# Optimization experiments

Hardware: AMD Instinct MI355X
Metric: run time of the kernel (lower is better)

Reference implementation:

```python
import jax, jax.numpy as jnp
import numpy as np

DIM = 2048
HEAD_DIM = 128
N_HEADS = 16
N_KV = 4
THETA = 10000.0
M = 2
B = 2
S = 2048


def _rope_table(seq_len, head_dim, theta):
    half = head_dim // 2
    inv_freq = 1.0 / (theta ** (jnp.arange(half, dtype=jnp.float32) * 2.0 / head_dim))
    ang = jnp.outer(jnp.arange(seq_len, dtype=jnp.float32), inv_freq)  # [S, half]
    cos, sin = jnp.cos(ang), jnp.sin(ang)
    # [S, half, 2, 2] rotation matrices: [[cos, -sin], [sin, cos]]
    return jnp.stack([jnp.stack([cos, -sin], axis=-1), jnp.stack([sin, cos], axis=-1)], axis=-2)


def setup_inputs() -> dict:
    key = jax.random.key(0)
    ks = jax.random.split(key, 6)
    std = DIM ** -0.5
    x = jax.random.normal(ks[0], (B, S, DIM), jnp.float32)
    Wq = jax.random.normal(ks[1], (M, DIM, N_HEADS * HEAD_DIM), jnp.float32) * std
    Wk = jax.random.normal(ks[2], (M, M, DIM, N_KV * HEAD_DIM), jnp.float32) * std
    Wv = jax.random.normal(ks[3], (M, M, DIM, N_KV * HEAD_DIM), jnp.float32) * std
    Wo = jax.random.normal(ks[4], (M, N_HEADS * HEAD_DIM, DIM), jnp.float32) * std
    modality_ids = jax.random.randint(ks[5], (B, S), 0, M, dtype=jnp.int32)
    freq_cis = _rope_table(S, HEAD_DIM, THETA)
    return {"x": x, "freq_cis": freq_cis, "Wq": Wq, "Wk": Wk, "Wv": Wv, "Wo": Wo,
            "modality_ids": modality_ids}


def _select_by_modality(all_proj, mid):
    # all_proj: [B, S, M, E]; mid: [B, S] int -> [B, S, E]
    Bb, Ss, Mm, E = all_proj.shape
    idx = jnp.broadcast_to(mid[:, :, None, None].astype(jnp.int32), (Bb, Ss, 1, E))
    return jnp.take_along_axis(all_proj, idx, axis=2)[:, :, 0]


def reference(x, freq_cis, Wq, Wk, Wv, Wo, modality_ids):
    Bb, Ss, D = x.shape
    mid = modality_ids

    # Per-modality Q projection, then per-token selection (gather/scatter in torch).
    q_all = jnp.einsum('bsd,mde->bsme', x, Wq)  # [B,S,M,H*hd]
    xq = _select_by_modality(q_all, mid)

    # In the original, xk[src token] accumulates wk[src_to_tgt](x) over ALL tgt,
    # which by linearity equals x @ sum_tgt(Wk[src, tgt]).
    Wk_sum = Wk.sum(axis=1)  # [M, D, Kh*hd]
    Wv_sum = Wv.sum(axis=1)
    k_all = jnp.einsum('bsd,mde->bsme', x, Wk_sum)
    v_all = jnp.einsum('bsd,mde->bsme', x, Wv_sum)
    xk = _select_by_modality(k_all, mid)
    xv = _select_by_modality(v_all, mid)

    xq = xq.reshape(Bb, Ss, N_HEADS, HEAD_DIM)
    xk = xk.reshape(Bb, Ss, N_KV, HEAD_DIM)
    xv = xv.reshape(Bb, Ss, N_KV, HEAD_DIM)

    # RoPE (positions = arange since tok_idx is None)
    F = freq_cis[:Ss]  # [S, hd/2, 2, 2]

    def rope(t):
        th = t.reshape(t.shape[0], t.shape[1], t.shape[2], HEAD_DIM // 2, 2)
        return jnp.einsum('bshdp,sdpq->bshdq', th, F).reshape(t.shape)

    xq = rope(xq)
    xk = rope(xk)

    # GQA repeat (interleaved, matching expand+reshape)
    rep = N_HEADS // N_KV
    xk = jnp.repeat(xk, rep, axis=2)
    xv = jnp.repeat(xv, rep, axis=2)

    q = xq.transpose(0, 2, 1, 3)  # [B,H,S,hd]
    k = xk.transpose(0, 2, 1, 3)
    v = xv.transpose(0, 2, 1, 3)

    scale = 1.0 / jnp.sqrt(jnp.asarray(HEAD_DIM, dtype=q.dtype))
    scores = jnp.einsum('bhqd,bhkd->bhqk', q, k) * scale
    attn = jax.nn.softmax(scores, axis=-1)
    out = jnp.einsum('bhqk,bhkd->bqhd', attn, v).reshape(Bb, Ss, N_HEADS * HEAD_DIM)

    # Per-modality output projection + selection
    o_all = jnp.einsum('bse,med->bsmd', out, Wo)  # [B,S,M,D]
    final = _select_by_modality(o_all, mid)
    return final
```

## Files before the change

kernel.cpp:

```cpp
#include <hip/hip_runtime.h>
#include <hip/hip_bf16.h>
#include <stdint.h>

typedef unsigned short u16;
typedef __attribute__((ext_vector_type(8))) __bf16 bf16x8;
typedef __attribute__((ext_vector_type(4))) float f32x4;
typedef __attribute__((ext_vector_type(16))) float f32x16;
typedef __attribute__((ext_vector_type(8))) u16 us8;
typedef __attribute__((ext_vector_type(4))) unsigned u32x4;

#define QSCALE 0.08838834764831843f

__device__ __forceinline__ u16 f2bf(float f) {
  unsigned u = __float_as_uint(f);
  u += 0x7fffu + ((u >> 16) & 1u);
  return (u16)(u >> 16);
}
__device__ __forceinline__ float bf2f(u16 h) {
  return __uint_as_float(((unsigned)h) << 16);
}
__device__ __forceinline__ void gload16(const void* g, void* l) {
  __builtin_amdgcn_global_load_lds(
      (const __attribute__((address_space(1))) unsigned int*)g,
      (__attribute__((address_space(3))) unsigned int*)l, 16, 0, 0);
}
__device__ __forceinline__ unsigned sx32(unsigned v) {
  return (unsigned)__shfl_xor((int)v, 32, 64);
}

__global__ __launch_bounds__(256) void wprep(
    const float* __restrict__ Wq, const float* __restrict__ Wk,
    const float* __restrict__ Wv, const float* __restrict__ Wo,
    u16* __restrict__ WCT, u16* __restrict__ WOT) {
  const int sec = blockIdx.z;
  const float* s0;
  const float* s1 = nullptr;
  u16* dst;
  int N;
  switch (sec) {
    case 0: s0 = Wq;                 dst = WCT;               N = 2048; break;
    case 1: s0 = Wq + 2048*2048;     dst = WCT + 2048*2048;   N = 2048; break;
    case 2: s0 = Wk;                 s1 = Wk + 2048*512;      dst = WCT + 4096*2048; N = 512; break;
    case 3: s0 = Wk + 2*2048*512;    s1 = Wk + 3*2048*512;    dst = WCT + 4608*2048; N = 512; break;
    case 4: s0 = Wv;                 s1 = Wv + 2048*512;      dst = WCT + 5120*2048; N = 512; break;
    case 5: s0 = Wv + 2*2048*512;    s1 = Wv + 3*2048*512;    dst = WCT + 5632*2048; N = 512; break;
    case 6: s0 = Wo;                 dst = WOT;               N = 2048; break;
    default: s0 = Wo + 2048*2048;    dst = WOT + 2048*2048;   N = 2048; break;
  }
  const int n0 = blockIdx.x * 32;
  if (n0 >= N) return;
  const int k0 = blockIdx.y * 32;
  __shared__ float tile[32][33];
  const int tx = threadIdx.x & 31, ty = threadIdx.x >> 5;
#pragma unroll
  for (int i = 0; i < 4; ++i) {
    int k = k0 + ty + 8 * i;
    float v = s0[(size_t)k * N + n0 + tx];
    if (s1) v += s1[(size_t)k * N + n0 + tx];
    tile[ty + 8 * i][tx] = v;
  }
  __syncthreads();
#pragma unroll
  for (int i = 0; i < 4; ++i) {
    int n = n0 + ty + 8 * i;
    dst[(size_t)n * 2048 + k0 + tx] = f2bf(tile[tx][ty + 8 * i]);
  }
}

__global__ __launch_bounds__(256) void xcast(const float* __restrict__ x,
                                             u16* __restrict__ Xbf) {
  size_t base = ((size_t)blockIdx.x * 256 + threadIdx.x) * 8;
  float4 a = *(const float4*)&x[base];
  float4 c = *(const float4*)&x[base + 4];
  us8 o;
  o[0] = f2bf(a.x); o[1] = f2bf(a.y); o[2] = f2bf(a.z); o[3] = f2bf(a.w);
  o[4] = f2bf(c.x); o[5] = f2bf(c.y); o[6] = f2bf(c.z); o[7] = f2bf(c.w);
  *(us8*)&Xbf[base] = o;
}

__global__ __launch_bounds__(256) void gemm_bt(
    const u16* __restrict__ A, const u16* __restrict__ B, u16* __restrict__ C,
    int Mdim, int Ndim, int Kdim) {
  __shared__ u16 As[128 * 32];
  __shared__ u16 Bs[128 * 32];
  const int nbx = gridDim.x;
  const int nwg = nbx * gridDim.y;
  int bid = blockIdx.y * nbx + blockIdx.x;
  const int q = nwg >> 3;
  int swz = (bid & 7) * q + (bid >> 3);
  const int bx = swz % nbx, by = swz / nbx;
  const int row0 = by * 128, col0 = bx * 128;
  const int tid = threadIdx.x, wid = tid >> 6, lane = tid & 63;
  const int lr = lane & 15, lg = lane >> 4;
  const int wr = wid >> 1, wc = wid & 1;
  const u16* Abase = A + (size_t)row0 * Kdim;
  const u16* Bbase = B + (size_t)col0 * Kdim;

  f32x4 acc[4][4];
#pragma unroll
  for (int m = 0; m < 4; ++m)
#pragma unroll
    for (int n = 0; n < 4; ++n)
#pragma unroll
      for (int r = 0; r < 4; ++r) acc[m][n][r] = 0.f;

  for (int k0 = 0; k0 < Kdim; k0 += 32) {
#pragma unroll
    for (int j = 0; j < 2; ++j) {
      int c = j * 256 + wid * 64 + lane;
      int r = c >> 2, g = c & 3;
      gload16(Abase + (size_t)r * Kdim + k0 + g * 8, &As[(j * 256 + wid * 64) * 8]);
      gload16(Bbase + (size_t)r * Kdim + k0 + g * 8, &Bs[(j * 256 + wid * 64) * 8]);
    }
    __syncthreads();
    bf16x8 af[4], bfr[4];
#pragma unroll
    for (int m = 0; m < 4; ++m)
      af[m] = *(const bf16x8*)&As[(64 * wr + 16 * m + lr) * 32 + 8 * lg];
#pragma unroll
    for (int n = 0; n < 4; ++n)
      bfr[n] = *(const bf16x8*)&Bs[(64 * wc + 16 * n + lr) * 32 + 8 * lg];
#pragma unroll
    for (int m = 0; m < 4; ++m)
#pragma unroll
      for (int n = 0; n < 4; ++n)
        acc[m][n] = __builtin_amdgcn_mfma_f32_16x16x32_bf16(af[m], bfr[n], acc[m][n], 0, 0, 0);
    __syncthreads();
  }
#pragma unroll
  for (int m = 0; m < 4; ++m)
#pragma unroll
    for (int n = 0; n < 4; ++n)
#pragma unroll
      for (int r = 0; r < 4; ++r) {
        int grow = row0 + 64 * wr + 16 * m + 4 * lg + r;
        int gcol = col0 + 64 * wc + 16 * n + lr;
        C[(size_t)grow * Ndim + gcol] = f2bf(acc[m][n][r]);
      }
}

__global__ __launch_bounds__(256) void gemm_out(
    const u16* __restrict__ A, const u16* __restrict__ B,
    const int* __restrict__ mid, float* __restrict__ out) {
  __shared__ u16 As[128 * 32];
  __shared__ u16 Bs[128 * 32];
  const int nbx = gridDim.x;
  const int nwg = nbx * gridDim.y;
  int bid = blockIdx.y * nbx + blockIdx.x;
  const int q = nwg >> 3;
  int swz = (bid & 7) * q + (bid >> 3);
  const int bx = swz % nbx, by = swz / nbx;
  const int row0 = by * 128, col0 = bx * 128;
  const int tid = threadIdx.x, wid = tid >> 6, lane = tid & 63;
  const int lr = lane & 15, lg = lane >> 4;
  const int wr = wid >> 1, wc = wid & 1;
  const u16* Abase = A + (size_t)row0 * 2048;
  const u16* Bbase = B + (size_t)col0 * 2048;

  f32x4 acc[4][4];
#pragma unroll
  for (int m = 0; m < 4; ++m)
#pragma unroll
    for (int n = 0; n < 4; ++n)
#pragma unroll
      for (int r = 0; r < 4; ++r) acc[m][n][r] = 0.f;

  for (int k0 = 0; k0 < 2048; k0 += 32) {
#pragma unroll
    for (int j = 0; j < 2; ++j) {
      int c = j * 256 + wid * 64 + lane;
      int r = c >> 2, g = c & 3;
      gload16(Abase + (size_t)r * 2048 + k0 + g * 8, &As[(j * 256 + wid * 64) * 8]);
      gload16(Bbase + (size_t)r * 2048 + k0 + g * 8, &Bs[(j * 256 + wid * 64) * 8]);
    }
    __syncthreads();
    bf16x8 af[4], bfr[4];
#pragma unroll
    for (int m = 0; m < 4; ++m)
      af[m] = *(const bf16x8*)&As[(64 * wr + 16 * m + lr) * 32 + 8 * lg];
#pragma unroll
    for (int n = 0; n < 4; ++n)
      bfr[n] = *(const bf16x8*)&Bs[(64 * wc + 16 * n + lr) * 32 + 8 * lg];
#pragma unroll
    for (int m = 0; m < 4; ++m)
#pragma unroll
      for (int n = 0; n < 4; ++n)
        acc[m][n] = __builtin_amdgcn_mfma_f32_16x16x32_bf16(af[m], bfr[n], acc[m][n], 0, 0, 0);
    __syncthreads();
  }
#pragma unroll
  for (int m = 0; m < 4; ++m)
#pragma unroll
    for (int n = 0; n < 4; ++n)
#pragma unroll
      for (int r = 0; r < 4; ++r) {
        int grow = row0 + 64 * wr + 16 * m + 4 * lg + r;
        int gcol = col0 + 64 * wc + 16 * n + lr;
        int mod = gcol >> 11;
        if (mid[grow] == mod)
          out[(size_t)grow * 2048 + (gcol & 2047)] = acc[m][n][r];
      }
}

__global__ __launch_bounds__(256) void rope_select(
    const u16* __restrict__ QKV, const int* __restrict__ mid,
    const float* __restrict__ fc, u16* __restrict__ Qr, u16* __restrict__ Kr) {
  const int t = blockIdx.x;
  const int b = t >> 11, s = t & 2047;
  const int m = mid[t];
  __shared__ float Fs[256];
  Fs[threadIdx.x] = fc[(size_t)s * 256 + threadIdx.x];
  __syncthreads();
  const int tid = threadIdx.x;
  {
    int p0 = tid * 4;
    int h = p0 >> 6, ph0 = p0 & 63;
    const u16* src = QKV + (size_t)t * 6144 + m * 2048 + h * 128 + 2 * ph0;
    us8 v = *(const us8*)src;
    us8 o;
#pragma unroll
    for (int j = 0; j < 4; ++j) {
      float x0 = bf2f(v[2 * j]), x1 = bf2f(v[2 * j + 1]);
      const float* F = &Fs[(ph0 + j) * 4];
      o[2 * j]     = f2bf((x0 * F[0] + x1 * F[2]) * QSCALE);
      o[2 * j + 1] = f2bf((x0 * F[1] + x1 * F[3]) * QSCALE);
    }
    *(us8*)(Qr + (((size_t)(b * 16 + h) * 2048) + s) * 128 + 2 * ph0) = o;
  }
  if (tid < 64) {
    int p0 = tid * 4;
    int kh = p0 >> 6, ph0 = p0 & 63;
    const u16* src = QKV + (size_t)t * 6144 + 4096 + m * 512 + kh * 128 + 2 * ph0;
    us8 v = *(const us8*)src;
    us8 o;
#pragma unroll
    for (int j = 0; j < 4; ++j) {
      float x0 = bf2f(v[2 * j]), x1 = bf2f(v[2 * j + 1]);
      const float* F = &Fs[(ph0 + j) * 4];
      o[2 * j]     = f2bf(x0 * F[0] + x1 * F[2]);
      o[2 * j + 1] = f2bf(x0 * F[1] + x1 * F[3]);
    }
    *(us8*)(Kr + (((size_t)(b * 4 + kh) * 2048) + s) * 128 + 2 * ph0) = o;
  }
}

__global__ __launch_bounds__(256) void vtrans(
    const u16* __restrict__ QKV, const int* __restrict__ mid, u16* __restrict__ Vt) {
  __shared__ u16 tilebuf[32][34];
  const int s0 = blockIdx.x * 32, d0 = blockIdx.y * 32, b = blockIdx.z;
  const int tx = threadIdx.x & 31, ty = threadIdx.x >> 5;
#pragma unroll
  for (int i = 0; i < 4; ++i) {
    int s = s0 + ty + 8 * i;
    int t = b * 2048 + s;
    int m = mid[t];
    tilebuf[ty + 8 * i][tx] = QKV[(size_t)t * 6144 + 5120 + m * 512 + d0 + tx];
  }
  __syncthreads();
#pragma unroll
  for (int i = 0; i < 4; ++i) {
    int d = d0 + ty + 8 * i;
    Vt[(((size_t)(b * 4 + (d >> 7)) * 128) + (d & 127)) * 2048 + s0 + tx] =
        tilebuf[tx][ty + 8 * i];
  }
}

__global__ __launch_bounds__(512, 2) void attn(
    const u16* __restrict__ Qr, const u16* __restrict__ Kr,
    const u16* __restrict__ Vt, u16* __restrict__ AO) {
  __shared__ u16 smem[34816];
  u16* Kbuf[2] = { smem,          smem + 16384 };
  u16* Vbuf[2] = { smem +  8192,  smem + 24576 };
  Kbuf[0] = smem;          Vbuf[0] = smem + 8192;
  Kbuf[1] = smem + 16384;  Vbuf[1] = smem + 24576;

  const int qt = blockIdx.x, hd = blockIdx.y, b = blockIdx.z;
  const int kvh = hd >> 2;
  const int tid = threadIdx.x, wid = tid >> 6;
  const int l31 = tid & 31, h = (tid >> 5) & 1;
  const bool hi = h != 0;

  const u16* qp = Qr + (((size_t)(b * 16 + hd) * 2048) + qt * 256 + wid * 32 + l31) * 128;
  const u16* kp = Kr + ((size_t)(b * 4 + kvh) * 2048) * 128;
  const u16* vp = Vt + ((size_t)(b * 4 + kvh) * 128) * 2048;

  bf16x8 qf[8];
#pragma unroll
  for (int ds = 0; ds < 8; ++ds)
    qf[ds] = *(const bf16x8*)(qp + 16 * ds + 8 * h);

  f32x16 oacc[4];
#pragma unroll
  for (int dt = 0; dt < 4; ++dt)
#pragma unroll
    for (int r = 0; r < 16; ++r) oacc[dt][r] = 0.f;
  float mrun = -1e30f, lrun = 0.f;

#define STAGE_KV(KB, DK, DV)                                                   \
  {                                                                            \
    _Pragma("unroll") for (int j = 0; j < 2; ++j) {                            \
      int c = j * 512 + tid;                                                   \
      int rk = c >> 4, gk = (c & 15) ^ (rk & 7);                               \
      gload16(kp + (size_t)((KB) + rk) * 128 + gk * 8,                         \
              (DK) + (j * 512 + wid * 64) * 8);                                \
      int rv = c >> 3, gv = (c & 7) ^ (rv & 7);                                \
      gload16(vp + (size_t)rv * 2048 + (KB) + gv * 8,                          \
              (DV) + (j * 512 + wid * 64) * 8);                                \
    }                                                                          \
  }

  STAGE_KV(0, Kbuf[0], Vbuf[0]);
  __syncthreads();

  int cur = 0;
  for (int kb = 0; kb < 2048; kb += 64) {
    const u16* Kb = Kbuf[cur];
    const u16* Vb = Vbuf[cur];
    if (kb + 64 < 2048) STAGE_KV(kb + 64, Kbuf[cur ^ 1], Vbuf[cur ^ 1]);

    f32x16 s0, s1;
#pragma unroll
    for (int r = 0; r < 16; ++r) { s0[r] = 0.f; s1[r] = 0.f; }
    const int key0 = l31, key1 = 32 + l31;
#pragma unroll
    for (int ds = 0; ds < 8; ++ds) {
      bf16x8 kf0 = *(const bf16x8*)&Kb[key0 * 128 + (((2 * ds + h) ^ (key0 & 7)) * 8)];
      s0 = __builtin_amdgcn_mfma_f32_32x32x16_bf16(kf0, qf[ds], s0, 0, 0, 0);
      bf16x8 kf1 = *(const bf16x8*)&Kb[key1 * 128 + (((2 * ds + h) ^ (key1 & 7)) * 8)];
      s1 = __builtin_amdgcn_mfma_f32_32x32x16_bf16(kf1, qf[ds], s1, 0, 0, 0);
    }

    float pm = -1e30f;
#pragma unroll
    for (int r = 0; r < 16; ++r) pm = fmaxf(pm, fmaxf(s0[r], s1[r]));
    pm = fmaxf(pm, __shfl_xor(pm, 32, 64));
    if (!__all(pm <= mrun + 8.f)) {
      float mn = fmaxf(mrun, pm);
      float sc = __expf(mrun - mn);
      mrun = mn;
      lrun *= sc;
#pragma unroll
      for (int dt = 0; dt < 4; ++dt)
#pragma unroll
        for (int r = 0; r < 16; ++r) oacc[dt][r] *= sc;
    }
    float ls = 0.f;
#pragma unroll
    for (int r = 0; r < 16; ++r) { s0[r] = __expf(s0[r] - mrun); ls += s0[r]; }
#pragma unroll
    for (int r = 0; r < 16; ++r) { s1[r] = __expf(s1[r] - mrun); ls += s1[r]; }
    ls += __shfl_xor(ls, 32, 64);
    lrun += ls;

    unsigned c[16];
#pragma unroll
    for (int j = 0; j < 8; ++j) {
      asm("v_cvt_pk_bf16_f32 %0, %1, %2" : "=v"(c[j]) : "v"(s0[2 * j]), "v"(s0[2 * j + 1]));
      asm("v_cvt_pk_bf16_f32 %0, %1, %2" : "=v"(c[8 + j]) : "v"(s1[2 * j]), "v"(s1[2 * j + 1]));
    }

#pragma unroll
    for (int st = 0; st < 4; ++st) {
      unsigned w0 = sx32(c[4 * st + 0]);
      unsigned w1 = sx32(c[4 * st + 1]);
      unsigned w2 = sx32(c[4 * st + 2]);
      unsigned w3 = sx32(c[4 * st + 3]);
      u32x4 pw;
      pw.x = hi ? w2 : c[4 * st + 0];
      pw.y = hi ? w3 : c[4 * st + 1];
      pw.z = hi ? c[4 * st + 2] : w0;
      pw.w = hi ? c[4 * st + 3] : w1;
      union { u32x4 u; bf16x8 bf; } pc;
      pc.u = pw;
#pragma unroll
      for (int dt = 0; dt < 4; ++dt) {
        int d = 32 * dt + l31;
        bf16x8 vf = *(const bf16x8*)&Vb[d * 64 + (((2 * st + h) ^ (d & 7)) * 8)];
        oacc[dt] = __builtin_amdgcn_mfma_f32_32x32x16_bf16(vf, pc.bf, oacc[dt], 0, 0, 0);
      }
    }
    __syncthreads();
    cur ^= 1;
  }

  u16* Os = smem;
  const float inv = 1.0f / lrun;
  const int q = wid * 32 + l31;
#pragma unroll
  for (int dt = 0; dt < 4; ++dt)
#pragma unroll
    for (int a = 0; a < 4; ++a) {
      int d = 32 * dt + 8 * a + 4 * h;
      ushort4 w;
      w.x = f2bf(oacc[dt][4 * a + 0] * inv);
      w.y = f2bf(oacc[dt][4 * a + 1] * inv);
      w.z = f2bf(oacc[dt][4 * a + 2] * inv);
      w.w = f2bf(oacc[dt][4 * a + 3] * inv);
      *(ushort4*)&Os[q * 136 + d] = w;
    }
  __syncthreads();
  const size_t orow = (size_t)b * 2048 + qt * 256;
#pragma unroll
  for (int rep = 0; rep < 8; ++rep) {
    int idx = rep * 512 + tid;
    int qq = idx >> 4, g = idx & 15;
    us8 v = *(const us8*)&Os[qq * 136 + g * 8];
    *(us8*)&AO[(orow + qq) * 2048 + hd * 128 + g * 8] = v;
  }
#undef STAGE_KV
}

extern "C" void kernel_launch(void* const* d_in, const int* in_sizes, int n_in,
                              void* d_out, int out_size, void* d_ws, size_t ws_size,
                              hipStream_t stream) {
  const float* x  = (const float*)d_in[0];
  const float* fc = (const float*)d_in[1];
  const float* Wq = (const float*)d_in[2];
  const float* Wk = (const float*)d_in[3];
  const float* Wv = (const float*)d_in[4];
  const float* Wo = (const float*)d_in[5];
  const int* mid  = (const int*)d_in[6];
  float* out = (float*)d_out;
  char* ws = (char*)d_ws;

  u16* XBF = (u16*)(ws);
  u16* WCT = (u16*)(ws + 16777216);
  u16* WOT = (u16*)(ws + 41943040);
  u16* QKV = (u16*)(ws + 58720256);
  u16* QR  = (u16*)(ws + 109051904);
  u16* KR  = (u16*)(ws + 125829120);
  u16* VT  = (u16*)(ws + 130023424);
  u16* AO  = (u16*)(ws + 134217728);
  if (ws_size < 150994944) return;

  wprep<<<dim3(64, 64, 8), dim3(256), 0, stream>>>(Wq, Wk, Wv, Wo, WCT, WOT);
  xcast<<<dim3(4096), dim3(256), 0, stream>>>(x, XBF);
  gemm_bt<<<dim3(48, 32), dim3(256), 0, stream>>>(XBF, WCT, QKV, 4096, 6144, 2048);
  rope_select<<<dim3(4096), dim3(256), 0, stream>>>(QKV, mid, fc, QR, KR);
  vtrans<<<dim3(64, 16, 2), dim3(256), 0, stream>>>(QKV, mid, VT);
  attn<<<dim3(8, 16, 2), dim3(512), 0, stream>>>(QR, KR, VT, AO);
  gemm_out<<<dim3(32, 32), dim3(256), 0, stream>>>(AO, WOT, mid, out);
}
```

Before: 540.0 us.

## Group tokens by modality and run only the matching projection per token

Adds count and scatter kernels that build a permutation sorting tokens by modality, then gathers rows through that permutation so each token is multiplied only by its own modality's Q/K/V and output weights. This halves GEMM FLOPs and the size of the QKV intermediate compared with computing every modality and discarding the unused one. The costs are two small extra launches, an atomic-based scatter, indirect row loads, and up to one partially empty tile per segment. Rope, V transpose and the output store now index through the permutation.

```diff
diff --git a/kernel.cpp b/kernel.cpp
--- a/kernel.cpp
+++ b/kernel.cpp
@@ -38,14 +38,14 @@
   u16* dst;
   int N;
   switch (sec) {
-    case 0: s0 = Wq;                 dst = WCT;               N = 2048; break;
-    case 1: s0 = Wq + 2048*2048;     dst = WCT + 2048*2048;   N = 2048; break;
-    case 2: s0 = Wk;                 s1 = Wk + 2048*512;      dst = WCT + 4096*2048; N = 512; break;
-    case 3: s0 = Wk + 2*2048*512;    s1 = Wk + 3*2048*512;    dst = WCT + 4608*2048; N = 512; break;
-    case 4: s0 = Wv;                 s1 = Wv + 2048*512;      dst = WCT + 5120*2048; N = 512; break;
-    case 5: s0 = Wv + 2*2048*512;    s1 = Wv + 3*2048*512;    dst = WCT + 5632*2048; N = 512; break;
-    case 6: s0 = Wo;                 dst = WOT;               N = 2048; break;
-    default: s0 = Wo + 2048*2048;    dst = WOT + 2048*2048;   N = 2048; break;
+    case 0: s0 = Wq;                 dst = WCT;                    N = 2048; break;
+    case 1: s0 = Wq + 2048*2048;     dst = WCT + (size_t)3072*2048; N = 2048; break;
+    case 2: s0 = Wk;                 s1 = Wk + 2048*512;  dst = WCT + (size_t)2048*2048; N = 512; break;
+    case 3: s0 = Wk + 2*2048*512;    s1 = Wk + 3*2048*512; dst = WCT + (size_t)5120*2048; N = 512; break;
+    case 4: s0 = Wv;                 s1 = Wv + 2048*512;  dst = WCT + (size_t)2560*2048; N = 512; break;
+    case 5: s0 = Wv + 2*2048*512;    s1 = Wv + 3*2048*512; dst = WCT + (size_t)5632*2048; N = 512; break;
+    case 6: s0 = Wo;                 dst = WOT;                    N = 2048; break;
+    default: s0 = Wo + 2048*2048;    dst = WOT + (size_t)2048*2048; N = 2048; break;
   }
   const int n0 = blockIdx.x * 32;
   if (n0 >= N) return;
@@ -78,23 +78,59 @@
   *(us8*)&Xbf[base] = o;
 }
 
-__global__ __launch_bounds__(256) void gemm_bt(
-    const u16* __restrict__ A, const u16* __restrict__ B, u16* __restrict__ C,
-    int Mdim, int Ndim, int Kdim) {
+__global__ __launch_bounds__(256) void scount(const int* __restrict__ mid,
+                                              int* __restrict__ cnt) {
+  __shared__ int sh[256];
+  int s = 0;
+  for (int i = threadIdx.x; i < 4096; i += 256) s += (mid[i] == 0);
+  sh[threadIdx.x] = s;
+  __syncthreads();
+  for (int o = 128; o; o >>= 1) {
+    if (threadIdx.x < o) sh[threadIdx.x] += sh[threadIdx.x + o];
+    __syncthreads();
+  }
+  if (threadIdx.x == 0) { cnt[0] = sh[0]; cnt[1] = 0; cnt[2] = 0; }
+}
+
+__global__ __launch_bounds__(256) void sscatter(const int* __restrict__ mid,
+                                                int* __restrict__ cnt,
+                                                int* __restrict__ perm,
+                                                int* __restrict__ inv) {
+  int t = blockIdx.x * 256 + threadIdx.x;
+  int m = mid[t];
+  int base = m ? cnt[0] : 0;
+  int pos = base + atomicAdd(&cnt[1 + m], 1);
+  perm[pos] = t;
+  inv[t] = pos;
+}
+
+__global__ __launch_bounds__(256) void gemm_qkv(
+    const u16* __restrict__ A, const u16* __restrict__ W, u16* __restrict__ Cq,
+    const int* __restrict__ cnt, const int* __restrict__ perm) {
   __shared__ u16 As[128 * 32];
   __shared__ u16 Bs[128 * 32];
-  const int nbx = gridDim.x;
-  const int nwg = nbx * gridDim.y;
+  const int n0 = cnt[0];
+  const int nbx = 24, nwg = 24 * 66;
   int bid = blockIdx.y * nbx + blockIdx.x;
-  const int q = nwg >> 3;
-  int swz = (bid & 7) * q + (bid >> 3);
+  const int q8 = nwg >> 3;
+  int swz = (bid & 7) * q8 + (bid >> 3);
   const int bx = swz % nbx, by = swz / nbx;
-  const int row0 = by * 128, col0 = bx * 128;
+  int seg, r0, rend;
+  if (by < 33) { seg = 0; r0 = by * 128; rend = n0; }
+  else         { seg = 1; r0 = n0 + (by - 33) * 128; rend = 4096; }
+  if (r0 >= rend) return;
+  const int col0 = bx * 128;
   const int tid = threadIdx.x, wid = tid >> 6, lane = tid & 63;
   const int lr = lane & 15, lg = lane >> 4;
   const int wr = wid >> 1, wc = wid & 1;
-  const u16* Abase = A + (size_t)row0 * Kdim;
-  const u16* Bbase = B + (size_t)col0 * Kdim;
+  const u16* W0 = W + ((size_t)seg * 3072 + col0) * 2048;
+  const int ra = tid >> 2, gA = tid & 3;
+  int ti0 = r0 + ra;      if (ti0 > rend - 1) ti0 = rend - 1;
+  int ti1 = r0 + 64 + ra; if (ti1 > rend - 1) ti1 = rend - 1;
+  const u16* Ar0 = A + (size_t)perm[ti0] * 2048;
+  const u16* Ar1 = A + (size_t)perm[ti1] * 2048;
+  const u16* Br0 = W0 + (size_t)ra * 2048;
+  const u16* Br1 = W0 + (size_t)(64 + ra) * 2048;
 
   f32x4 acc[4][4];
 #pragma unroll
@@ -104,14 +140,11 @@
 #pragma unroll
       for (int r = 0; r < 4; ++r) acc[m][n][r] = 0.f;
 
-  for (int k0 = 0; k0 < Kdim; k0 += 32) {
-#pragma unroll
-    for (int j = 0; j < 2; ++j) {
-      int c = j * 256 + wid * 64 + lane;
-      int r = c >> 2, g = c & 3;
-      gload16(Abase + (size_t)r * Kdim + k0 + g * 8, &As[(j * 256 + wid * 64) * 8]);
-      gload16(Bbase + (size_t)r * Kdim + k0 + g * 8, &Bs[(j * 256 + wid * 64) * 8]);
-    }
+  for (int k0 = 0; k0 < 2048; k0 += 32) {
+    gload16(Ar0 + k0 + gA * 8, &As[(0 * 256 + wid * 64) * 8]);
+    gload16(Br0 + k0 + gA * 8, &Bs[(0 * 256 + wid * 64) * 8]);
+    gload16(Ar1 + k0 + gA * 8, &As[(1 * 256 + wid * 64) * 8]);
+    gload16(Br1 + k0 + gA * 8, &Bs[(1 * 256 + wid * 64) * 8]);
     __syncthreads();
     bf16x8 af[4], bfr[4];
 #pragma unroll
@@ -133,29 +166,42 @@
     for (int n = 0; n < 4; ++n)
 #pragma unroll
       for (int r = 0; r < 4; ++r) {
-        int grow = row0 + 64 * wr + 16 * m + 4 * lg + r;
-        int gcol = col0 + 64 * wc + 16 * n + lr;
-        C[(size_t)grow * Ndim + gcol] = f2bf(acc[m][n][r]);
+        int grow = r0 + 64 * wr + 16 * m + 4 * lg + r;
+        if (grow < rend) {
+          int gcol = col0 + 64 * wc + 16 * n + lr;
+          Cq[(size_t)grow * 3072 + gcol] = f2bf(acc[m][n][r]);
+        }
       }
 }
 
 __global__ __launch_bounds__(256) void gemm_out(
-    const u16* __restrict__ A, const u16* __restrict__ B,
-    const int* __restrict__ mid, float* __restrict__ out) {
+    const u16* __restrict__ A, const u16* __restrict__ W,
+    const int* __restrict__ cnt, const int* __restrict__ perm,
+    float* __restrict__ out) {
   __shared__ u16 As[128 * 32];
   __shared__ u16 Bs[128 * 32];
-  const int nbx = gridDim.x;
-  const int nwg = nbx * gridDim.y;
+  const int n0 = cnt[0];
+  const int nbx = 16, nwg = 16 * 66;
   int bid = blockIdx.y * nbx + blockIdx.x;
-  const int q = nwg >> 3;
-  int swz = (bid & 7) * q + (bid >> 3);
+  const int q8 = nwg >> 3;
+  int swz = (bid & 7) * q8 + (bid >> 3);
   const int bx = swz % nbx, by = swz / nbx;
-  const int row0 = by * 128, col0 = bx * 128;
+  int seg, r0, rend;
+  if (by < 33) { seg = 0; r0 = by * 128; rend = n0; }
+  else         { seg = 1; r0 = n0 + (by - 33) * 128; rend = 4096; }
+  if (r0 >= rend) return;
+  const int col0 = bx * 128;
   const int tid = threadIdx.x, wid = tid >> 6, lane = tid & 63;
   const int lr = lane & 15, lg = lane >> 4;
   const int wr = wid >> 1, wc = wid & 1;
-  const u16* Abase = A + (size_t)row0 * 2048;
-  const u16* Bbase = B + (size_t)col0 * 2048;
+  const u16* W0 = W + ((size_t)seg * 2048 + col0) * 2048;
+  const int ra = tid >> 2, gA = tid & 3;
+  int ti0 = r0 + ra;      if (ti0 > rend - 1) ti0 = rend - 1;
+  int ti1 = r0 + 64 + ra; if (ti1 > rend - 1) ti1 = rend - 1;
+  const u16* Ar0 = A + (size_t)perm[ti0] * 2048;
+  const u16* Ar1 = A + (size_t)perm[ti1] * 2048;
+  const u16* Br0 = W0 + (size_t)ra * 2048;
+  const u16* Br1 = W0 + (size_t)(64 + ra) * 2048;
 
   f32x4 acc[4][4];
 #pragma unroll
@@ -166,13 +212,10 @@
       for (int r = 0; r < 4; ++r) acc[m][n][r] = 0.f;
 
   for (int k0 = 0; k0 < 2048; k0 += 32) {
-#pragma unroll
-    for (int j = 0; j < 2; ++j) {
-      int c = j * 256 + wid * 64 + lane;
-      int r = c >> 2, g = c & 3;
-      gload16(Abase + (size_t)r * 2048 + k0 + g * 8, &As[(j * 256 + wid * 64) * 8]);
-      gload16(Bbase + (size_t)r * 2048 + k0 + g * 8, &Bs[(j * 256 + wid * 64) * 8]);
-    }
+    gload16(Ar0 + k0 + gA * 8, &As[(0 * 256 + wid * 64) * 8]);
+    gload16(Br0 + k0 + gA * 8, &Bs[(0 * 256 + wid * 64) * 8]);
+    gload16(Ar1 + k0 + gA * 8, &As[(1 * 256 + wid * 64) * 8]);
+    gload16(Br1 + k0 + gA * 8, &Bs[(1 * 256 + wid * 64) * 8]);
     __syncthreads();
     bf16x8 af[4], bfr[4];
 #pragma unroll
@@ -191,23 +234,25 @@
 #pragma unroll
   for (int m = 0; m < 4; ++m)
 #pragma unroll
-    for (int n = 0; n < 4; ++n)
-#pragma unroll
-      for (int r = 0; r < 4; ++r) {
-        int grow = row0 + 64 * wr + 16 * m + 4 * lg + r;
-        int gcol = col0 + 64 * wc + 16 * n + lr;
-        int mod = gcol >> 11;
-        if (mid[grow] == mod)
-          out[(size_t)grow * 2048 + (gcol & 2047)] = acc[m][n][r];
+    for (int r = 0; r < 4; ++r) {
+      int grow = r0 + 64 * wr + 16 * m + 4 * lg + r;
+      if (grow < rend) {
+        int tok = perm[grow];
+#pragma unroll
+        for (int n = 0; n < 4; ++n) {
+          int gcol = col0 + 64 * wc + 16 * n + lr;
+          out[(size_t)tok * 2048 + gcol] = acc[m][n][r];
+        }
       }
+    }
 }
 
 __global__ __launch_bounds__(256) void rope_select(
-    const u16* __restrict__ QKV, const int* __restrict__ mid,
+    const u16* __restrict__ QKVs, const int* __restrict__ perm,
     const float* __restrict__ fc, u16* __restrict__ Qr, u16* __restrict__ Kr) {
-  const int t = blockIdx.x;
+  const int i = blockIdx.x;
+  const int t = perm[i];
   const int b = t >> 11, s = t & 2047;
-  const int m = mid[t];
   __shared__ float Fs[256];
   Fs[threadIdx.x] = fc[(size_t)s * 256 + threadIdx.x];
   __syncthreads();
@@ -215,7 +260,7 @@
   {
     int p0 = tid * 4;
     int h = p0 >> 6, ph0 = p0 & 63;
-    const u16* src = QKV + (size_t)t * 6144 + m * 2048 + h * 128 + 2 * ph0;
+    const u16* src = QKVs + (size_t)i * 3072 + h * 128 + 2 * ph0;
     us8 v = *(const us8*)src;
     us8 o;
 #pragma unroll
@@ -230,7 +275,7 @@
   if (tid < 64) {
     int p0 = tid * 4;
     int kh = p0 >> 6, ph0 = p0 & 63;
-    const u16* src = QKV + (size_t)t * 6144 + 4096 + m * 512 + kh * 128 + 2 * ph0;
+    const u16* src = QKVs + (size_t)i * 3072 + 2048 + kh * 128 + 2 * ph0;
     us8 v = *(const us8*)src;
     us8 o;
 #pragma unroll
@@ -245,16 +290,15 @@
 }
 
 __global__ __launch_bounds__(256) void vtrans(
-    const u16* __restrict__ QKV, const int* __restrict__ mid, u16* __restrict__ Vt) {
+    const u16* __restrict__ QKVs, const int* __restrict__ inv, u16* __restrict__ Vt) {
   __shared__ u16 tilebuf[32][34];
   const int s0 = blockIdx.x * 32, d0 = blockIdx.y * 32, b = blockIdx.z;
   const int tx = threadIdx.x & 31, ty = threadIdx.x >> 5;
 #pragma unroll
   for (int i = 0; i < 4; ++i) {
     int s = s0 + ty + 8 * i;
-    int t = b * 2048 + s;
-    int m = mid[t];
-    tilebuf[ty + 8 * i][tx] = QKV[(size_t)t * 6144 + 5120 + m * 512 + d0 + tx];
+    int row = inv[b * 2048 + s];
+    tilebuf[ty + 8 * i][tx] = QKVs[(size_t)row * 3072 + 2560 + d0 + tx];
   }
   __syncthreads();
 #pragma unroll
@@ -269,8 +313,8 @@
     const u16* __restrict__ Qr, const u16* __restrict__ Kr,
     const u16* __restrict__ Vt, u16* __restrict__ AO) {
   __shared__ u16 smem[34816];
-  u16* Kbuf[2] = { smem,          smem + 16384 };
-  u16* Vbuf[2] = { smem +  8192,  smem + 24576 };
+  u16* Kbuf[2];
+  u16* Vbuf[2];
   Kbuf[0] = smem;          Vbuf[0] = smem + 8192;
   Kbuf[1] = smem + 16384;  Vbuf[1] = smem + 24576;
 
@@ -423,21 +467,26 @@
   float* out = (float*)d_out;
   char* ws = (char*)d_ws;
 
-  u16* XBF = (u16*)(ws);
-  u16* WCT = (u16*)(ws + 16777216);
-  u16* WOT = (u16*)(ws + 41943040);
-  u16* QKV = (u16*)(ws + 58720256);
-  u16* QR  = (u16*)(ws + 109051904);
-  u16* KR  = (u16*)(ws + 125829120);
-  u16* VT  = (u16*)(ws + 130023424);
-  u16* AO  = (u16*)(ws + 134217728);
+  u16* XBF  = (u16*)(ws);
+  u16* WCT  = (u16*)(ws + 16777216);
+  u16* WOT  = (u16*)(ws + 41943040);
+  u16* QKVs = (u16*)(ws + 58720256);
+  u16* QR   = (u16*)(ws + 83886080);
+  u16* KR   = (u16*)(ws + 100663296);
+  u16* VT   = (u16*)(ws + 104857600);
+  u16* AO   = (u16*)(ws + 109051904);
+  int* perm = (int*)(ws + 125829120);
+  int* inv  = (int*)(ws + 125845504);
+  int* cnt  = (int*)(ws + 125861888);
   if (ws_size < 150994944) return;
 
   wprep<<<dim3(64, 64, 8), dim3(256), 0, stream>>>(Wq, Wk, Wv, Wo, WCT, WOT);
   xcast<<<dim3(4096), dim3(256), 0, stream>>>(x, XBF);
-  gemm_bt<<<dim3(48, 32), dim3(256), 0, stream>>>(XBF, WCT, QKV, 4096, 6144, 2048);
-  rope_select<<<dim3(4096), dim3(256), 0, stream>>>(QKV, mid, fc, QR, KR);
-  vtrans<<<dim3(64, 16, 2), dim3(256), 0, stream>>>(QKV, mid, VT);
+  scount<<<dim3(1), dim3(256), 0, stream>>>(mid, cnt);
+  sscatter<<<dim3(16), dim3(256), 0, stream>>>(mid, cnt, perm, inv);
+  gemm_qkv<<<dim3(24, 66), dim3(256), 0, stream>>>(XBF, WCT, QKVs, cnt, perm);
+  rope_select<<<dim3(4096), dim3(256), 0, stream>>>(QKVs, perm, fc, QR, KR);
+  vtrans<<<dim3(64, 16, 2), dim3(256), 0, stream>>>(QKVs, inv, VT);
   attn<<<dim3(8, 16, 2), dim3(512), 0, stream>>>(QR, KR, VT, AO);
-  gemm_out<<<dim3(32, 32), dim3(256), 0, stream>>>(AO, WOT, mid, out);
-}
+  gemm_out<<<dim3(16, 66), dim3(256), 0, stream>>>(AO, WOT, cnt, perm, out);
+}
```

Result: slower. 629.4 us (+16.6%).
